# Kernel optimization log

Measured on AMD Instinct MI355X. Metric: run time of the kernel, lower is better.

Reference implementation:

```python
import jax, jax.numpy as jnp
import numpy as np

DIM_V = 512
H = 8
EPS = 1e-5

def _layernorm(x, g, b):
    mu = jnp.mean(x, axis=-1, keepdims=True)
    var = jnp.var(x, axis=-1, keepdims=True)
    return (x - mu) * jax.lax.rsqrt(var + EPS) * g + b

def setup_inputs() -> dict:
    key = jax.random.key(0)
    ks = jax.random.split(key, 10)
    B, Nq, Nk, dq, dk, dv = 8, 1024, 1024, 512, 512, DIM_V
    def lin(k, fan_in, shape):
        bound = 1.0 / np.sqrt(fan_in)
        return jax.random.uniform(k, shape, jnp.float32, -bound, bound)
    return {
        "Q": jax.random.normal(ks[0], (B, Nq, dq), jnp.float32),
        "K": jax.random.normal(ks[1], (B, Nk, dk), jnp.float32),
        "Wq": lin(ks[2], dq, (dv, dq)), "bq": lin(ks[3], dq, (dv,)),
        "Wk": lin(ks[4], dk, (dv, dk)), "bk": lin(ks[5], dk, (dv,)),
        "Wv": lin(ks[6], dk, (dv, dk)), "bv": lin(ks[7], dk, (dv,)),
        "Wo": lin(ks[8], dv, (dv, dv)), "bo": lin(ks[9], dv, (dv,)),
        "g0": jnp.ones((dv,), jnp.float32), "beta0": jnp.zeros((dv,), jnp.float32),
        "g1": jnp.ones((dv,), jnp.float32), "beta1": jnp.zeros((dv,), jnp.float32),
    }

def reference(Q, K, Wq, bq, Wk, bk, Wv, bv, Wo, bo, g0, beta0, g1, beta1):
    B, Nq, _ = Q.shape
    Nk = K.shape[1]
    d_h = DIM_V // H
    Qp = Q @ Wq.T + bq            # [B,Nq,dv]
    Kp = K @ Wk.T + bk            # [B,Nk,dv]
    Vp = K @ Wv.T + bv            # [B,Nk,dv]
    # split heads along feature dim (matches torch split(dim_split,2)+cat(0))
    Qh = Qp.reshape(B, Nq, H, d_h).transpose(0, 2, 1, 3)  # [B,H,Nq,dh]
    Kh = Kp.reshape(B, Nk, H, d_h).transpose(0, 2, 1, 3)
    Vh = Vp.reshape(B, Nk, H, d_h).transpose(0, 2, 1, 3)
    # NOTE: original scales by sqrt(dim_V), the FULL model dim
    scores = jnp.einsum('bhnd,bhmd->bhnm', Qh, Kh) / jnp.sqrt(jnp.float32(DIM_V))
    A = jax.nn.softmax(scores, axis=-1)                   # [B,H,Nq,Nk]
    Oh = Qh + jnp.einsum('bhnm,bhmd->bhnd', A, Vh)        # residual on projected Q
    O = Oh.transpose(0, 2, 1, 3).reshape(B, Nq, DIM_V)
    O = _layernorm(O, g0, beta0)
    O = O + jax.nn.relu(O @ Wo.T + bo)
    O = _layernorm(O, g1, beta1)
    return O
```

## Files before the change

### kernel.cpp

```cpp
#include <hip/hip_runtime.h>
#include <hip/hip_bf16.h>

typedef __hip_bfloat16 bf16;
typedef short bf16x8 __attribute__((ext_vector_type(8)));
typedef float f32x4 __attribute__((ext_vector_type(4)));
typedef unsigned int u32;

static __device__ __forceinline__ float bfu2f(unsigned short u) { return __uint_as_float((u32)u << 16); }
static __device__ __forceinline__ u32 pack2(float a, float b) {
    return (u32)__bfloat16_as_ushort(__float2bfloat16(a))
         | ((u32)__bfloat16_as_ushort(__float2bfloat16(b)) << 16);
}
static __device__ __forceinline__ float wave_sum(float v) {
    #pragma unroll
    for (int off = 32; off > 0; off >>= 1) v += __shfl_xor(v, off);
    return v;
}

__global__ __launch_bounds__(256) void castall(const float* __restrict__ Q,  const float* __restrict__ K,
                                               const float* __restrict__ Wq, const float* __restrict__ Wk,
                                               const float* __restrict__ Wv, const float* __restrict__ Wo,
                                               bf16* __restrict__ dQ,  bf16* __restrict__ dK,
                                               bf16* __restrict__ dWq, bf16* __restrict__ dWk,
                                               bf16* __restrict__ dWv, bf16* __restrict__ dWo)
{
    const int b = blockIdx.x;
    const float* src; bf16* dst; size_t off;
    if (b < 1024)      { src = Q;  dst = dQ;  off = (size_t)b * 4096; }
    else if (b < 2048) { src = K;  dst = dK;  off = (size_t)(b - 1024) * 4096; }
    else {
        const int wb = b - 2048, wi = wb >> 6;
        off = (size_t)(wb & 63) * 4096;
        src = wi == 0 ? Wq : wi == 1 ? Wk : wi == 2 ? Wv : Wo;
        dst = wi == 0 ? dWq : wi == 1 ? dWk : wi == 2 ? dWv : dWo;
    }
    const size_t p = off + threadIdx.x * 16;
    const float4 v0 = *(const float4*)(src + p);
    const float4 v1 = *(const float4*)(src + p + 4);
    const float4 v2 = *(const float4*)(src + p + 8);
    const float4 v3 = *(const float4*)(src + p + 12);
    uint4 o0, o1;
    o0.x = pack2(v0.x, v0.y); o0.y = pack2(v0.z, v0.w);
    o0.z = pack2(v1.x, v1.y); o0.w = pack2(v1.z, v1.w);
    o1.x = pack2(v2.x, v2.y); o1.y = pack2(v2.z, v2.w);
    o1.z = pack2(v3.x, v3.y); o1.w = pack2(v3.z, v3.w);
    *(uint4*)(dst + p)     = o0;
    *(uint4*)(dst + p + 8) = o1;
}

#define LDSK 40

__global__ __launch_bounds__(256) void gemm_qkv(const bf16* __restrict__ Aq, const bf16* __restrict__ Ak,
                                                const bf16* __restrict__ Wq, const bf16* __restrict__ Wk,
                                                const bf16* __restrict__ Wv,
                                                const float* __restrict__ bq, const float* __restrict__ bk,
                                                const float* __restrict__ bv,
                                                bf16* __restrict__ oQ, bf16* __restrict__ oK,
                                                bf16* __restrict__ oV)
{
    __shared__ bf16 As[128 * LDSK];
    __shared__ bf16 Bs[128 * LDSK];

    const int tid = threadIdx.x, lane = tid & 63, wave = tid >> 6;
    const int yy = blockIdx.y, wi = yy >> 2;
    const bf16* A     = wi == 0 ? Aq : Ak;
    const bf16* W     = wi == 0 ? Wq : wi == 1 ? Wk : Wv;
    const float* bias = wi == 0 ? bq : wi == 1 ? bk : bv;
    bf16* out         = wi == 0 ? oQ : wi == 1 ? oK : oV;
    const int mode    = wi == 2 ? 2 : 1;
    const int bm = blockIdx.x * 128;
    const int bn = (yy & 3) * 128;

    const int lrow = tid >> 2, lcol = (tid & 3) * 8;
    const int wm = (wave >> 1) * 64, wn = (wave & 1) * 64;
    const int fr = lane & 15, kq = (lane >> 4) * 8;

    f32x4 acc[4][4] = {};
    const bf16* Ap = A + (size_t)(bm + lrow) * 512 + lcol;
    const bf16* Wp = W + (size_t)(bn + lrow) * 512 + lcol;

    for (int k0 = 0; k0 < 512; k0 += 32) {
        const int4 av0 = *(const int4*)(Ap + k0);
        const int4 av1 = *(const int4*)(Ap + k0 + (size_t)64 * 512);
        const int4 wv0 = *(const int4*)(Wp + k0);
        const int4 wv1 = *(const int4*)(Wp + k0 + (size_t)64 * 512);
        __syncthreads();
        *(int4*)(&As[lrow * LDSK + lcol])        = av0;
        *(int4*)(&As[(lrow + 64) * LDSK + lcol]) = av1;
        *(int4*)(&Bs[lrow * LDSK + lcol])        = wv0;
        *(int4*)(&Bs[(lrow + 64) * LDSK + lcol]) = wv1;
        __syncthreads();

        bf16x8 fa[4], fb[4];
        #pragma unroll
        for (int i = 0; i < 4; i++) {
            fa[i] = *(const bf16x8*)(&As[(wm + 16 * i + fr) * LDSK + kq]);
            fb[i] = *(const bf16x8*)(&Bs[(wn + 16 * i + fr) * LDSK + kq]);
        }
        #pragma unroll
        for (int i = 0; i < 4; i++)
            #pragma unroll
            for (int j = 0; j < 4; j++)
                acc[i][j] = __builtin_amdgcn_mfma_f32_16x16x32_bf16(fa[i], fb[j], acc[i][j], 0, 0, 0);
    }

    const int r0 = (lane >> 4) * 4;
    #pragma unroll
    for (int i = 0; i < 4; i++) {
        #pragma unroll
        for (int j = 0; j < 4; j++) {
            const int col = bn + wn + 16 * j + fr;
            const float bv2 = bias[col];
            #pragma unroll
            for (int r = 0; r < 4; r++) {
                const int row = bm + wm + 16 * i + r0 + r;
                const float v = acc[i][j][r] + bv2;
                const int b = row >> 10, n = row & 1023;
                const int h = col >> 6,  d = col & 63;
                size_t idx;
                if (mode == 1) idx = ((size_t)(b * 8 + h) * 1024 + n) * 64 + d;
                else           idx = ((size_t)(b * 8 + h) * 64 + d) * 1024 + n;
                out[idx] = __float2bfloat16(v);
            }
        }
    }
}

__global__ __launch_bounds__(256) void gemm_o(const bf16* __restrict__ A,
                                              const bf16* __restrict__ W,
                                              const float* __restrict__ bias,
                                              bf16* __restrict__ out)
{
    __shared__ bf16 As[64 * LDSK];
    __shared__ bf16 Bs[128 * LDSK];

    const int tid = threadIdx.x, lane = tid & 63, wave = tid >> 6;
    const int bm = blockIdx.x * 64;
    const int bn = blockIdx.y * 128;

    const int lrow = tid >> 2, lcol = (tid & 3) * 8;
    const int wn = wave * 32;
    const int fr = lane & 15, kq = (lane >> 4) * 8;

    f32x4 acc[4][2] = {};
    const bf16* Ap = A + (size_t)(bm + (lrow & 63)) * 512 + lcol;
    const bf16* Wp = W + (size_t)(bn + lrow) * 512 + lcol;

    for (int k0 = 0; k0 < 512; k0 += 32) {
        const int4 av  = *(const int4*)(Ap + k0);
        const int4 wv0 = *(const int4*)(Wp + k0);
        const int4 wv1 = *(const int4*)(Wp + k0 + (size_t)64 * 512);
        __syncthreads();
        *(int4*)(&As[(lrow & 63) * LDSK + lcol]) = av;
        *(int4*)(&Bs[lrow * LDSK + lcol])        = wv0;
        *(int4*)(&Bs[(lrow + 64) * LDSK + lcol]) = wv1;
        __syncthreads();

        bf16x8 fa[4], fb[2];
        #pragma unroll
        for (int i = 0; i < 4; i++)
            fa[i] = *(const bf16x8*)(&As[(16 * i + fr) * LDSK + kq]);
        #pragma unroll
        for (int j = 0; j < 2; j++)
            fb[j] = *(const bf16x8*)(&Bs[(wn + 16 * j + fr) * LDSK + kq]);
        #pragma unroll
        for (int i = 0; i < 4; i++)
            #pragma unroll
            for (int j = 0; j < 2; j++)
                acc[i][j] = __builtin_amdgcn_mfma_f32_16x16x32_bf16(fa[i], fb[j], acc[i][j], 0, 0, 0);
    }

    const int r0 = (lane >> 4) * 4;
    #pragma unroll
    for (int i = 0; i < 4; i++) {
        #pragma unroll
        for (int j = 0; j < 2; j++) {
            const int col = bn + wn + 16 * j + fr;
            const float bv = bias[col];
            #pragma unroll
            for (int r = 0; r < 4; r++) {
                const int row = bm + 16 * i + r0 + r;
                out[(size_t)row * 512 + col] = __float2bfloat16(acc[i][j][r] + bv);
            }
        }
    }
}

__global__ __launch_bounds__(256) void attn_mfma(const bf16* __restrict__ Qh,
                                                 const bf16* __restrict__ Kh,
                                                 const bf16* __restrict__ VhT,
                                                 bf16* __restrict__ Oc)
{
    __shared__ bf16 Ks[64 * 72];
    __shared__ bf16 Vs[64 * 72];
    __shared__ bf16 Ps[4][16 * 72];

    const int tid = threadIdx.x, lane = tid & 63, w = tid >> 6;
    const int bh = blockIdx.y;
    const int wq = blockIdx.x * 64 + w * 16;

    const bf16* Qb = Qh  + ((size_t)bh * 1024 + wq) * 64;
    const bf16* Kb = Kh  + (size_t)bh * 1024 * 64;
    const bf16* Vb = VhT + (size_t)bh * 64 * 1024;

    const int fl = lane & 15, fq = lane >> 4;

    bf16x8 qf0 = *(const bf16x8*)(Qb + fl * 64 + fq * 8);
    bf16x8 qf1 = *(const bf16x8*)(Qb + fl * 64 + 32 + fq * 8);

    f32x4 o[4] = {};
    float lsum = 0.f;
    const float sc2 = 0.04419417382415922f * 1.4426950408889634f;

    const int srow = tid >> 3;
    const int seq  = tid & 7;

    for (int kt = 0; kt < 16; kt++) {
        const int m0 = kt * 64;
        const int4 kv0 = *(const int4*)(Kb + (size_t)(m0 + srow) * 64 + seq * 8);
        const int4 kv1 = *(const int4*)(Kb + (size_t)(m0 + srow + 32) * 64 + seq * 8);
        const int4 vv0 = *(const int4*)(Vb + (size_t)srow * 1024 + m0 + seq * 8);
        const int4 vv1 = *(const int4*)(Vb + (size_t)(srow + 32) * 1024 + m0 + seq * 8);
        __syncthreads();
        *(int4*)(&Ks[srow * 72 + seq * 8])        = kv0;
        *(int4*)(&Ks[(srow + 32) * 72 + seq * 8]) = kv1;
        *(int4*)(&Vs[srow * 72 + seq * 8])        = vv0;
        *(int4*)(&Vs[(srow + 32) * 72 + seq * 8]) = vv1;
        __syncthreads();

        f32x4 st[4] = {};
        #pragma unroll
        for (int tm = 0; tm < 4; tm++) {
            bf16x8 kf0 = *(const bf16x8*)(&Ks[(16 * tm + fl) * 72 + fq * 8]);
            bf16x8 kf1 = *(const bf16x8*)(&Ks[(16 * tm + fl) * 72 + 32 + fq * 8]);
            st[tm] = __builtin_amdgcn_mfma_f32_16x16x32_bf16(kf0, qf0, st[tm], 0, 0, 0);
            st[tm] = __builtin_amdgcn_mfma_f32_16x16x32_bf16(kf1, qf1, st[tm], 0, 0, 0);
        }

        #pragma unroll
        for (int tm = 0; tm < 4; tm++) {
            float p0 = __builtin_amdgcn_exp2f(st[tm][0] * sc2);
            float p1 = __builtin_amdgcn_exp2f(st[tm][1] * sc2);
            float p2 = __builtin_amdgcn_exp2f(st[tm][2] * sc2);
            float p3 = __builtin_amdgcn_exp2f(st[tm][3] * sc2);
            lsum += (p0 + p1) + (p2 + p3);
            uint2 pk;
            pk.x = pack2(p0, p1);
            pk.y = pack2(p2, p3);
            *(uint2*)(&Ps[w][fl * 72 + 16 * tm + fq * 4]) = pk;
        }

        bf16x8 pf0 = *(const bf16x8*)(&Ps[w][fl * 72 + fq * 8]);
        bf16x8 pf1 = *(const bf16x8*)(&Ps[w][fl * 72 + 32 + fq * 8]);
        #pragma unroll
        for (int jd = 0; jd < 4; jd++) {
            bf16x8 vf0 = *(const bf16x8*)(&Vs[(16 * jd + fl) * 72 + fq * 8]);
            bf16x8 vf1 = *(const bf16x8*)(&Vs[(16 * jd + fl) * 72 + 32 + fq * 8]);
            o[jd] = __builtin_amdgcn_mfma_f32_16x16x32_bf16(vf0, pf0, o[jd], 0, 0, 0);
            o[jd] = __builtin_amdgcn_mfma_f32_16x16x32_bf16(vf1, pf1, o[jd], 0, 0, 0);
        }
    }

    lsum += __shfl_xor(lsum, 16);
    lsum += __shfl_xor(lsum, 32);
    const float linv = 1.f / lsum;

    const int b = bh >> 3, h = bh & 7;
    const size_t obase = ((size_t)(b * 1024 + wq + fl)) * 512 + h * 64;
    #pragma unroll
    for (int jd = 0; jd < 4; jd++) {
        const ushort4 qr = *(const ushort4*)(Qb + fl * 64 + 16 * jd + fq * 4);
        const float v0 = o[jd][0] * linv + bfu2f(qr.x);
        const float v1 = o[jd][1] * linv + bfu2f(qr.y);
        const float v2 = o[jd][2] * linv + bfu2f(qr.z);
        const float v3 = o[jd][3] * linv + bfu2f(qr.w);
        uint2 w2;
        w2.x = pack2(v0, v1);
        w2.y = pack2(v2, v3);
        *(uint2*)(&Oc[obase + 16 * jd + fq * 4]) = w2;
    }
}

__global__ __launch_bounds__(256) void ln0(const bf16* __restrict__ X,
                                           const float* __restrict__ g,
                                           const float* __restrict__ be,
                                           bf16* __restrict__ Y)
{
    const int lane = threadIdx.x & 63;
    const int row = blockIdx.x * 4 + (threadIdx.x >> 6);
    const size_t base = (size_t)row * 512 + lane * 8;
    const bf16x8 xv = *(const bf16x8*)(X + base);
    float x[8];
    #pragma unroll
    for (int j = 0; j < 8; j++) x[j] = bfu2f((unsigned short)xv[j]);
    float s = 0.f, s2 = 0.f;
    #pragma unroll
    for (int j = 0; j < 8; j++) { s += x[j]; s2 += x[j] * x[j]; }
    s = wave_sum(s); s2 = wave_sum(s2);
    const float mean = s * (1.f / 512.f);
    const float var = s2 * (1.f / 512.f) - mean * mean;
    const float rs = rsqrtf(fmaxf(var, 0.f) + 1e-5f);
    const float4 gv0 = *(const float4*)(g + lane * 8);
    const float4 gv1 = *(const float4*)(g + lane * 8 + 4);
    const float4 bv0 = *(const float4*)(be + lane * 8);
    const float4 bv1 = *(const float4*)(be + lane * 8 + 4);
    uint4 ov;
    ov.x = pack2((x[0]-mean)*rs*gv0.x + bv0.x, (x[1]-mean)*rs*gv0.y + bv0.y);
    ov.y = pack2((x[2]-mean)*rs*gv0.z + bv0.z, (x[3]-mean)*rs*gv0.w + bv0.w);
    ov.z = pack2((x[4]-mean)*rs*gv1.x + bv1.x, (x[5]-mean)*rs*gv1.y + bv1.y);
    ov.w = pack2((x[6]-mean)*rs*gv1.z + bv1.z, (x[7]-mean)*rs*gv1.w + bv1.w);
    *(uint4*)(Y + base) = ov;
}

__global__ __launch_bounds__(256) void ln1(const bf16* __restrict__ X,
                                           const bf16* __restrict__ R,
                                           const float* __restrict__ g,
                                           const float* __restrict__ be,
                                           float* __restrict__ Y)
{
    const int lane = threadIdx.x & 63;
    const int row = blockIdx.x * 4 + (threadIdx.x >> 6);
    const size_t base = (size_t)row * 512 + lane * 8;
    const bf16x8 xv = *(const bf16x8*)(X + base);
    const bf16x8 rv = *(const bf16x8*)(R + base);
    float x[8];
    #pragma unroll
    for (int j = 0; j < 8; j++)
        x[j] = bfu2f((unsigned short)rv[j]) + fmaxf(bfu2f((unsigned short)xv[j]), 0.f);
    float s = 0.f, s2 = 0.f;
    #pragma unroll
    for (int j = 0; j < 8; j++) { s += x[j]; s2 += x[j] * x[j]; }
    s = wave_sum(s); s2 = wave_sum(s2);
    const float mean = s * (1.f / 512.f);
    const float var = s2 * (1.f / 512.f) - mean * mean;
    const float rs = rsqrtf(fmaxf(var, 0.f) + 1e-5f);
    const float4 gv0 = *(const float4*)(g + lane * 8);
    const float4 gv1 = *(const float4*)(g + lane * 8 + 4);
    const float4 bv0 = *(const float4*)(be + lane * 8);
    const float4 bv1 = *(const float4*)(be + lane * 8 + 4);
    float4 y0, y1;
    y0.x = (x[0]-mean)*rs*gv0.x + bv0.x; y0.y = (x[1]-mean)*rs*gv0.y + bv0.y;
    y0.z = (x[2]-mean)*rs*gv0.z + bv0.z; y0.w = (x[3]-mean)*rs*gv0.w + bv0.w;
    y1.x = (x[4]-mean)*rs*gv1.x + bv1.x; y1.y = (x[5]-mean)*rs*gv1.y + bv1.y;
    y1.z = (x[6]-mean)*rs*gv1.z + bv1.z; y1.w = (x[7]-mean)*rs*gv1.w + bv1.w;
    *(float4*)(Y + base)     = y0;
    *(float4*)(Y + base + 4) = y1;
}

extern "C" void kernel_launch(void* const* d_in, const int* in_sizes, int n_in,
                              void* d_out, int out_size, void* d_ws, size_t ws_size,
                              hipStream_t stream)
{
    const float* Q   = (const float*)d_in[0];
    const float* K   = (const float*)d_in[1];
    const float* Wq  = (const float*)d_in[2];
    const float* bq  = (const float*)d_in[3];
    const float* Wk  = (const float*)d_in[4];
    const float* bk  = (const float*)d_in[5];
    const float* Wv  = (const float*)d_in[6];
    const float* bv  = (const float*)d_in[7];
    const float* Wo  = (const float*)d_in[8];
    const float* bo  = (const float*)d_in[9];
    const float* g0  = (const float*)d_in[10];
    const float* be0 = (const float*)d_in[11];
    const float* g1  = (const float*)d_in[12];
    const float* be1 = (const float*)d_in[13];
    float* out = (float*)d_out;

    const size_t NQK = (size_t)8 * 1024 * 512;
    const size_t NW  = (size_t)512 * 512;
    bf16* ws   = (bf16*)d_ws;
    bf16* cQ   = ws;
    bf16* cK   = cQ + NQK;
    bf16* cWq  = cK + NQK;
    bf16* cWk  = cWq + NW;
    bf16* cWv  = cWk + NW;
    bf16* cWo  = cWv + NW;
    bf16* pQh  = cWo + NW;
    bf16* pKh  = pQh + NQK;
    bf16* pVhT = pKh + NQK;
    bf16* pOc  = (bf16*)d_out;
    bf16* pO1  = pKh;
    bf16* pTmp = pQh;

    castall<<<2304, 256, 0, stream>>>(Q, K, Wq, Wk, Wv, Wo, cQ, cK, cWq, cWk, cWv, cWo);
    gemm_qkv<<<dim3(64, 12), 256, 0, stream>>>(cQ, cK, cWq, cWk, cWv, bq, bk, bv, pQh, pKh, pVhT);
    attn_mfma<<<dim3(16, 64), 256, 0, stream>>>(pQh, pKh, pVhT, pOc);
    ln0<<<2048, 256, 0, stream>>>(pOc, g0, be0, pO1);
    gemm_o<<<dim3(128, 4), 256, 0, stream>>>(pO1, cWo, bo, pTmp);
    ln1<<<2048, 256, 0, stream>>>(pTmp, pO1, g1, be1, out);
}
```

Before: 204.5 us.

## Load GEMM and attention tiles straight into LDS with XOR-swizzled layout

```diff
diff --git a/kernel.cpp b/kernel.cpp
--- a/kernel.cpp
+++ b/kernel.cpp
@@ -15,6 +15,12 @@
     #pragma unroll
     for (int off = 32; off > 0; off >>= 1) v += __shfl_xor(v, off);
     return v;
+}
+
+static __device__ __forceinline__ void gll16(const bf16* g, bf16* l) {
+    __builtin_amdgcn_global_load_lds((const __attribute__((address_space(1))) void*)g,
+                                     (__attribute__((address_space(3))) void*)l,
+                                     16, 0, 0);
 }
 
 __global__ __launch_bounds__(256) void castall(const float* __restrict__ Q,  const float* __restrict__ K,
@@ -48,8 +54,6 @@
     *(uint4*)(dst + p + 8) = o1;
 }
 
-#define LDSK 40
-
 __global__ __launch_bounds__(256) void gemm_qkv(const bf16* __restrict__ Aq, const bf16* __restrict__ Ak,
                                                 const bf16* __restrict__ Wq, const bf16* __restrict__ Wk,
                                                 const bf16* __restrict__ Wv,
@@ -58,8 +62,8 @@
                                                 bf16* __restrict__ oQ, bf16* __restrict__ oK,
                                                 bf16* __restrict__ oV)
 {
-    __shared__ bf16 As[128 * LDSK];
-    __shared__ bf16 Bs[128 * LDSK];
+    __shared__ bf16 As[128 * 32];
+    __shared__ bf16 Bs[128 * 32];
 
     const int tid = threadIdx.x, lane = tid & 63, wave = tid >> 6;
     const int yy = blockIdx.y, wi = yy >> 2;
@@ -71,31 +75,31 @@
     const int bm = blockIdx.x * 128;
     const int bn = (yy & 3) * 128;
 
-    const int lrow = tid >> 2, lcol = (tid & 3) * 8;
+    const int srow = tid >> 2;
+    const int sg8  = (((tid & 3) ^ (srow & 3)) * 8);
     const int wm = (wave >> 1) * 64, wn = (wave & 1) * 64;
-    const int fr = lane & 15, kq = (lane >> 4) * 8;
+    const int fr = lane & 15, fq = lane >> 4;
+    const int kqs = ((fq ^ (fr & 3)) * 8);
 
     f32x4 acc[4][4] = {};
-    const bf16* Ap = A + (size_t)(bm + lrow) * 512 + lcol;
-    const bf16* Wp = W + (size_t)(bn + lrow) * 512 + lcol;
+    const bf16* Ap = A + (size_t)(bm + srow) * 512 + sg8;
+    const bf16* Wp = W + (size_t)(bn + srow) * 512 + sg8;
+    bf16* AsD = As + 8 * tid;
+    bf16* BsD = Bs + 8 * tid;
 
     for (int k0 = 0; k0 < 512; k0 += 32) {
-        const int4 av0 = *(const int4*)(Ap + k0);
-        const int4 av1 = *(const int4*)(Ap + k0 + (size_t)64 * 512);
-        const int4 wv0 = *(const int4*)(Wp + k0);
-        const int4 wv1 = *(const int4*)(Wp + k0 + (size_t)64 * 512);
-        __syncthreads();
-        *(int4*)(&As[lrow * LDSK + lcol])        = av0;
-        *(int4*)(&As[(lrow + 64) * LDSK + lcol]) = av1;
-        *(int4*)(&Bs[lrow * LDSK + lcol])        = wv0;
-        *(int4*)(&Bs[(lrow + 64) * LDSK + lcol]) = wv1;
+        __syncthreads();
+        gll16(Ap + k0,                    AsD);
+        gll16(Ap + k0 + (size_t)64 * 512, AsD + 2048);
+        gll16(Wp + k0,                    BsD);
+        gll16(Wp + k0 + (size_t)64 * 512, BsD + 2048);
         __syncthreads();
 
         bf16x8 fa[4], fb[4];
         #pragma unroll
         for (int i = 0; i < 4; i++) {
-            fa[i] = *(const bf16x8*)(&As[(wm + 16 * i + fr) * LDSK + kq]);
-            fb[i] = *(const bf16x8*)(&Bs[(wn + 16 * i + fr) * LDSK + kq]);
+            fa[i] = *(const bf16x8*)(&As[(wm + 16 * i + fr) * 32 + kqs]);
+            fb[i] = *(const bf16x8*)(&Bs[(wn + 16 * i + fr) * 32 + kqs]);
         }
         #pragma unroll
         for (int i = 0; i < 4; i++)
@@ -104,7 +108,7 @@
                 acc[i][j] = __builtin_amdgcn_mfma_f32_16x16x32_bf16(fa[i], fb[j], acc[i][j], 0, 0, 0);
     }
 
-    const int r0 = (lane >> 4) * 4;
+    const int r0 = fq * 4;
     #pragma unroll
     for (int i = 0; i < 4; i++) {
         #pragma unroll
@@ -131,38 +135,39 @@
                                               const float* __restrict__ bias,
                                               bf16* __restrict__ out)
 {
-    __shared__ bf16 As[64 * LDSK];
-    __shared__ bf16 Bs[128 * LDSK];
+    __shared__ bf16 As[64 * 32];
+    __shared__ bf16 Bs[128 * 32];
 
     const int tid = threadIdx.x, lane = tid & 63, wave = tid >> 6;
     const int bm = blockIdx.x * 64;
     const int bn = blockIdx.y * 128;
 
-    const int lrow = tid >> 2, lcol = (tid & 3) * 8;
+    const int srow = tid >> 2;
+    const int sg8  = (((tid & 3) ^ (srow & 3)) * 8);
     const int wn = wave * 32;
-    const int fr = lane & 15, kq = (lane >> 4) * 8;
+    const int fr = lane & 15, fq = lane >> 4;
+    const int kqs = ((fq ^ (fr & 3)) * 8);
 
     f32x4 acc[4][2] = {};
-    const bf16* Ap = A + (size_t)(bm + (lrow & 63)) * 512 + lcol;
-    const bf16* Wp = W + (size_t)(bn + lrow) * 512 + lcol;
+    const bf16* Ap = A + (size_t)(bm + srow) * 512 + sg8;
+    const bf16* Wp = W + (size_t)(bn + srow) * 512 + sg8;
+    bf16* AsD = As + 8 * tid;
+    bf16* BsD = Bs + 8 * tid;
 
     for (int k0 = 0; k0 < 512; k0 += 32) {
-        const int4 av  = *(const int4*)(Ap + k0);
-        const int4 wv0 = *(const int4*)(Wp + k0);
-        const int4 wv1 = *(const int4*)(Wp + k0 + (size_t)64 * 512);
-        __syncthreads();
-        *(int4*)(&As[(lrow & 63) * LDSK + lcol]) = av;
-        *(int4*)(&Bs[lrow * LDSK + lcol])        = wv0;
-        *(int4*)(&Bs[(lrow + 64) * LDSK + lcol]) = wv1;
+        __syncthreads();
+        gll16(Ap + k0,                    AsD);
+        gll16(Wp + k0,                    BsD);
+        gll16(Wp + k0 + (size_t)64 * 512, BsD + 2048);
         __syncthreads();
 
         bf16x8 fa[4], fb[2];
         #pragma unroll
         for (int i = 0; i < 4; i++)
-            fa[i] = *(const bf16x8*)(&As[(16 * i + fr) * LDSK + kq]);
+            fa[i] = *(const bf16x8*)(&As[(16 * i + fr) * 32 + kqs]);
         #pragma unroll
         for (int j = 0; j < 2; j++)
-            fb[j] = *(const bf16x8*)(&Bs[(wn + 16 * j + fr) * LDSK + kq]);
+            fb[j] = *(const bf16x8*)(&Bs[(wn + 16 * j + fr) * 32 + kqs]);
         #pragma unroll
         for (int i = 0; i < 4; i++)
             #pragma unroll
@@ -170,7 +175,7 @@
                 acc[i][j] = __builtin_amdgcn_mfma_f32_16x16x32_bf16(fa[i], fb[j], acc[i][j], 0, 0, 0);
     }
 
-    const int r0 = (lane >> 4) * 4;
+    const int r0 = fq * 4;
     #pragma unroll
     for (int i = 0; i < 4; i++) {
         #pragma unroll
@@ -191,8 +196,8 @@
                                                  const bf16* __restrict__ VhT,
                                                  bf16* __restrict__ Oc)
 {
-    __shared__ bf16 Ks[64 * 72];
-    __shared__ bf16 Vs[64 * 72];
+    __shared__ bf16 Ks[64 * 64];
+    __shared__ bf16 Vs[64 * 64];
     __shared__ bf16 Ps[4][16 * 72];
 
     const int tid = threadIdx.x, lane = tid & 63, w = tid >> 6;
@@ -204,6 +209,9 @@
     const bf16* Vb = VhT + (size_t)bh * 64 * 1024;
 
     const int fl = lane & 15, fq = lane >> 4;
+    const int flk = fl & 7;
+    const int gA = (fq ^ flk) * 8;
+    const int gB = ((4 | fq) ^ flk) * 8;
 
     bf16x8 qf0 = *(const bf16x8*)(Qb + fl * 64 + fq * 8);
     bf16x8 qf1 = *(const bf16x8*)(Qb + fl * 64 + 32 + fq * 8);
@@ -213,26 +221,27 @@
     const float sc2 = 0.04419417382415922f * 1.4426950408889634f;
 
     const int srow = tid >> 3;
-    const int seq  = tid & 7;
+    const int sg8  = (((tid & 7) ^ (srow & 7)) * 8);
+    const bf16* KbR = Kb + (size_t)srow * 64 + sg8;
+    const bf16* VbR0 = Vb + (size_t)srow * 1024 + sg8;
+    const bf16* VbR1 = Vb + (size_t)(srow + 32) * 1024 + sg8;
+    bf16* KsD = Ks + 8 * tid;
+    bf16* VsD = Vs + 8 * tid;
 
     for (int kt = 0; kt < 16; kt++) {
         const int m0 = kt * 64;
-        const int4 kv0 = *(const int4*)(Kb + (size_t)(m0 + srow) * 64 + seq * 8);
-        const int4 kv1 = *(const int4*)(Kb + (size_t)(m0 + srow + 32) * 64 + seq * 8);
-        const int4 vv0 = *(const int4*)(Vb + (size_t)srow * 1024 + m0 + seq * 8);
-        const int4 vv1 = *(const int4*)(Vb + (size_t)(srow + 32) * 1024 + m0 + seq * 8);
-        __syncthreads();
-        *(int4*)(&Ks[srow * 72 + seq * 8])        = kv0;
-        *(int4*)(&Ks[(srow + 32) * 72 + seq * 8]) = kv1;
-        *(int4*)(&Vs[srow * 72 + seq * 8])        = vv0;
-        *(int4*)(&Vs[(srow + 32) * 72 + seq * 8]) = vv1;
+        __syncthreads();
+        gll16(KbR + (size_t)m0 * 64,        KsD);
+        gll16(KbR + (size_t)(m0 + 32) * 64, KsD + 2048);
+        gll16(VbR0 + m0,                    VsD);
+        gll16(VbR1 + m0,                    VsD + 2048);
         __syncthreads();
 
         f32x4 st[4] = {};
         #pragma unroll
         for (int tm = 0; tm < 4; tm++) {
-            bf16x8 kf0 = *(const bf16x8*)(&Ks[(16 * tm + fl) * 72 + fq * 8]);
-            bf16x8 kf1 = *(const bf16x8*)(&Ks[(16 * tm + fl) * 72 + 32 + fq * 8]);
+            bf16x8 kf0 = *(const bf16x8*)(&Ks[(16 * tm + fl) * 64 + gA]);
+            bf16x8 kf1 = *(const bf16x8*)(&Ks[(16 * tm + fl) * 64 + gB]);
             st[tm] = __builtin_amdgcn_mfma_f32_16x16x32_bf16(kf0, qf0, st[tm], 0, 0, 0);
             st[tm] = __builtin_amdgcn_mfma_f32_16x16x32_bf16(kf1, qf1, st[tm], 0, 0, 0);
         }
@@ -254,8 +263,8 @@
         bf16x8 pf1 = *(const bf16x8*)(&Ps[w][fl * 72 + 32 + fq * 8]);
         #pragma unroll
         for (int jd = 0; jd < 4; jd++) {
-            bf16x8 vf0 = *(const bf16x8*)(&Vs[(16 * jd + fl) * 72 + fq * 8]);
-            bf16x8 vf1 = *(const bf16x8*)(&Vs[(16 * jd + fl) * 72 + 32 + fq * 8]);
+            bf16x8 vf0 = *(const bf16x8*)(&Vs[(16 * jd + fl) * 64 + gA]);
+            bf16x8 vf1 = *(const bf16x8*)(&Vs[(16 * jd + fl) * 64 + gB]);
             o[jd] = __builtin_amdgcn_mfma_f32_16x16x32_bf16(vf0, pf0, o[jd], 0, 0, 0);
             o[jd] = __builtin_amdgcn_mfma_f32_16x16x32_bf16(vf1, pf1, o[jd], 0, 0, 0);
         }
```

Result: faster. 189.1 us (-7.5%).
